# Optimization experiments

Measured on AMD Instinct MI355X. Metric: run time of the kernel, lower is better.

Reference implementation:

```python
import jax, jax.numpy as jnp
import numpy as np

HEADS = 12
DIM_HEAD = 64
PATCHES = 196  # tokens_to_attend (space attention)
DIM = 768
BATCH = 8
FRAMES = 16
TOKENS = FRAMES * PATCHES + 1  # + CLS


def setup_inputs() -> dict:
    key = jax.random.key(0)
    k1, k2, k3 = jax.random.split(key, 3)
    x = jax.random.normal(k1, (BATCH, TOKENS, DIM), dtype=jnp.float32)
    # small init scale keeps softmax logits in a sane range
    W_qkv = jax.random.normal(k2, (DIM, 3 * HEADS * DIM_HEAD), dtype=jnp.float32) * 0.02
    W_0 = jax.random.normal(k3, (HEADS * DIM_HEAD, DIM), dtype=jnp.float32) * 0.02
    return {"x": x, "W_qkv": W_qkv, "W_0": W_0}


def _mhsa(q, k, v, scale):
    # q: [g,h,i,d], k/v: [g,h,j,d]
    s = jnp.einsum('ghid,ghjd->ghij', q, k) * scale
    a = jax.nn.softmax(s, axis=-1)
    return jnp.einsum('ghij,ghjd->ghid', a, v)


def reference(x, W_qkv, W_0):
    b, t, _ = x.shape
    h, dh, p = HEADS, DIM_HEAD, PATCHES
    scale = dh ** -0.5

    qkv = x @ W_qkv  # [b,t,dh*3*h], flattened in (d, k, h) order per einops pattern
    qkv = qkv.reshape(b, t, dh, 3, h)
    q = jnp.transpose(qkv[:, :, :, 0, :], (0, 3, 1, 2))  # [b,h,t,d]
    k = jnp.transpose(qkv[:, :, :, 1, :], (0, 3, 1, 2))
    v = jnp.transpose(qkv[:, :, :, 2, :], (0, 3, 1, 2))

    # CLS query attends over ALL space-time tokens
    cls_q, q3 = q[:, :, :1], q[:, :, 1:]
    out_cls = _mhsa(cls_q, k, v, scale)  # [b,h,1,d]

    cls_k, k3 = k[:, :, :1], k[:, :, 1:]
    cls_v, v3 = v[:, :, :1], v[:, :, 1:]

    f = (t - 1) // p  # frames

    def space_rearrange(z):  # 'b h (f p) d -> (b f) h p d'
        z = z.reshape(b, h, f, p, dh)
        return jnp.transpose(z, (0, 2, 1, 3, 4)).reshape(b * f, h, p, dh)

    q_sep = space_rearrange(q3)
    k_sep = space_rearrange(k3)
    v_sep = space_rearrange(v3)

    # broadcast CLS key/value to every frame group: 'b ... -> (b tile) ...'
    cls_k = jnp.repeat(cls_k, f, axis=0)  # [b*f,h,1,d]
    cls_v = jnp.repeat(cls_v, f, axis=0)

    kk = jnp.concatenate((cls_k, k_sep), axis=2)  # [b*f,h,p+1,d]
    vv = jnp.concatenate((cls_v, v_sep), axis=2)

    out_sp = _mhsa(q_sep, kk, vv, scale)  # [b*f,h,p,d]

    # merge: '(b f) h p d -> b h (f p) d' (space=True path)
    out_sp = out_sp.reshape(b, f, h, p, dh)
    out_sp = jnp.transpose(out_sp, (0, 2, 1, 3, 4)).reshape(b, h, f * p, dh)

    out = jnp.concatenate((out_cls, out_sp), axis=2)  # [b,h,t,d]
    out = jnp.transpose(out, (0, 2, 1, 3)).reshape(b, t, h * dh)
    return out @ W_0
```

## Files before the change

### kernel.cpp

```cpp
#include <hip/hip_runtime.h>
#include <hip/hip_bf16.h>
#include <cstdint>

typedef unsigned short u16;
typedef uint32_t u32;
typedef __attribute__((ext_vector_type(8))) u16 u16x8;
typedef __attribute__((ext_vector_type(4))) u16 u16x4;
typedef __attribute__((ext_vector_type(8))) __bf16 bf16x8;
typedef __attribute__((ext_vector_type(4))) float f32x4;

#define B_    8
#define T_    3137
#define H_    12
#define F_    16
#define D_    768
#define M1    25096
#define VSTR  3200
#define NSPL  16
#define SPK   208

__device__ __forceinline__ u16 f2bf(float f) {
  unsigned u = __float_as_uint(f);
  return (u16)((u + 0x7FFFu + ((u >> 16) & 1u)) >> 16);
}
__device__ __forceinline__ float b2f(u16 v) {
  return __uint_as_float(((unsigned)v) << 16);
}

#define GLL(g, l) __builtin_amdgcn_global_load_lds( \
    (const __attribute__((address_space(1))) void*)(g), \
    (__attribute__((address_space(3))) void*)(l), 16, 0, 0)

__device__ __forceinline__ void dsr(bf16x8& d, u32 abyte) {
  asm volatile("ds_read_b128 %0, %1" : "=v"(d) : "v"(abyte));
}

#define BARR  __builtin_amdgcn_s_barrier()
#define LGKM0 asm volatile("s_waitcnt lgkmcnt(0)")
#define SCB   __builtin_amdgcn_sched_barrier(0)
#define PRI1  __builtin_amdgcn_s_setprio(1)
#define PRI0  __builtin_amdgcn_s_setprio(0)

__global__ __launch_bounds__(256) void k_cvt_x(const float* __restrict__ x,
                                               u16* __restrict__ xb, int n4) {
  int i = blockIdx.x * 256 + threadIdx.x;
  if (i >= n4) return;
  float4 v = ((const float4*)x)[i];
  u16x4 o = { f2bf(v.x), f2bf(v.y), f2bf(v.z), f2bf(v.w) };
  *(u16x4*)(xb + (size_t)i * 4) = o;
}

__global__ __launch_bounds__(256) void k_transpose(const float* __restrict__ in,
                                                   u16* __restrict__ out,
                                                   int R, int C, int qkvperm) {
  __shared__ float tile[32][33];
  int c0 = blockIdx.x * 32, r0 = blockIdx.y * 32;
  int tx = threadIdx.x, ty = threadIdx.y;
  #pragma unroll
  for (int i = ty; i < 32; i += 8)
    tile[i][tx] = in[(size_t)(r0 + i) * C + c0 + tx];
  __syncthreads();
  #pragma unroll
  for (int i = ty; i < 32; i += 8) {
    int c = c0 + i;
    int orow;
    if (qkvperm) {
      int d = c / 36, rem = c - d * 36;
      int comp = rem / 12, hh = rem - comp * 12;
      orow = comp * 768 + hh * 64 + d;
    } else {
      orow = c;
    }
    out[(size_t)orow * R + r0 + tx] = f2bf(tile[tx][i]);
  }
}

template<int EPI, int NX>
__global__ __launch_bounds__(256, 2) void k_gemm(const u16* __restrict__ A,
                                                 const u16* __restrict__ Bm,
                                                 float* __restrict__ outF,
                                                 u16* __restrict__ Qb,
                                                 u16* __restrict__ Kb,
                                                 u16* __restrict__ Vt) {
  __shared__ u16 lds[32768];
  const int tid = threadIdx.x;
  const int lane = tid & 63;
  const int wid = tid >> 6;
  const int wr = wid >> 1, wc = wid & 1;
  const int li = lane & 15, lg = lane >> 4;

  const int nwg = NX * 197;
  const int q = nwg >> 3, r = nwg & 7;
  const int g = blockIdx.x;
  const int xcd = g & 7, pos = g >> 3;
  const int s = ((xcd < r) ? xcd * (q + 1) : r * (q + 1) + (xcd - r) * q) + pos;
  const int arow0 = (s / NX) * 128;
  const int brow0 = (s % NX) * 128;

  const int srow = wid * 32 + (lane >> 3);
  const int scol = ((lane & 7) ^ (lane >> 3)) * 8;
  const u16* gA = A  + (size_t)(arow0 + srow) * 768 + scol;
  const u16* gB = Bm + (size_t)(brow0 + srow) * 768 + scol;

  const u32 ldsb = (u32)(uintptr_t)(__attribute__((address_space(3))) u16*)(&lds[0]);
  const u32 e0 = (u32)((lg ^ (li & 7)) * 16);
  const u32 e1 = (u32)(((lg + 4) ^ (li & 7)) * 16);
  const u32 aA = ldsb + (u32)(wr * 64 + li) * 128;
  const u32 aB = ldsb + 16384 + (u32)(wc * 64 + li) * 128;

  f32x4 acc[4][4] = {};

#define STAGE(TB, KS) do { const int kb_ = (KS) * 64; \
    _Pragma("unroll") for (int c_ = 0; c_ < 4; ++c_) { \
      GLL(gA + kb_ + c_ * 8 * 768, lds + (TB) * 16384 + wid * 2048 + c_ * 512); \
      GLL(gB + kb_ + c_ * 8 * 768, lds + (TB) * 16384 + 8192 + wid * 2048 + c_ * 512); \
    } \
  } while (0)

#define STEP(CUR, KV) do { \
    { const int ks_ = ((KV) + 1 < 12) ? (KV) + 1 : 11; STAGE((CUR) ^ 1, ks_); } \
    asm volatile("s_waitcnt vmcnt(8)"); \
    BARR; \
    bf16x8 af[4][2], bfr[4][2]; \
    _Pragma("unroll") for (int m = 0; m < 4; ++m) { \
      dsr(af[m][0], aA + (CUR) * 32768 + m * 2048 + e0); \
      dsr(af[m][1], aA + (CUR) * 32768 + m * 2048 + e1); } \
    _Pragma("unroll") for (int n = 0; n < 4; ++n) { \
      dsr(bfr[n][0], aB + (CUR) * 32768 + n * 2048 + e0); \
      dsr(bfr[n][1], aB + (CUR) * 32768 + n * 2048 + e1); } \
    LGKM0; SCB; PRI1; \
    _Pragma("unroll") for (int m = 0; m < 4; ++m) \
    _Pragma("unroll") for (int n = 0; n < 4; ++n) { \
      acc[m][n] = __builtin_amdgcn_mfma_f32_16x16x32_bf16(af[m][0], bfr[n][0], acc[m][n], 0, 0, 0); \
      acc[m][n] = __builtin_amdgcn_mfma_f32_16x16x32_bf16(af[m][1], bfr[n][1], acc[m][n], 0, 0, 0); } \
    PRI0; BARR; \
  } while (0)

  STAGE(0, 0);

  #pragma unroll 1
  for (int kk = 0; kk < 12; kk += 2) {
    STEP(0, kk);
    STEP(1, kk + 1);
  }
#undef STAGE
#undef STEP

  if (EPI == 0) {
    #pragma unroll
    for (int m = 0; m < 4; ++m)
      #pragma unroll
      for (int n = 0; n < 4; ++n) {
        const int colp = brow0 + wc * 64 + n * 16 + li;
        #pragma unroll
        for (int rr = 0; rr < 4; ++rr) {
          const int row = arow0 + wr * 64 + m * 16 + lg * 4 + rr;
          if (row < M1)
            __builtin_nontemporal_store(acc[m][n][rr], outF + (size_t)row * 768 + colp);
        }
      }
  } else {
    const int comp = brow0 / 768;
    const float qsc = (comp == 0) ? 0.125f : 1.0f;
    const int b0r = arow0 / T_;
    const int RB = (b0r + 1) * T_;
    __syncthreads();
    if (comp < 2) {
      u16* tl = &lds[0];
      #pragma unroll
      for (int m = 0; m < 4; ++m)
        #pragma unroll
        for (int n = 0; n < 4; ++n)
          #pragma unroll
          for (int rr = 0; rr < 4; ++rr)
            tl[(wr * 64 + m * 16 + lg * 4 + rr) * 136 + wc * 64 + n * 16 + li] =
                f2bf(acc[m][n][rr] * qsc);
      __syncthreads();
      u16* dst = (comp == 0) ? Qb : Kb;
      const int hh0 = (brow0 - comp * 768) >> 6;
      const int grp = tid >> 4, li2 = tid & 15;
      #pragma unroll
      for (int pass = 0; pass < 16; ++pass) {
        const int idx = pass * 16 + grp;
        const int row = idx >> 1, hl = idx & 1;
        const int rg = arow0 + row;
        if (rg >= M1) continue;
        const int bb = (rg >= RB) ? b0r + 1 : b0r;
        const int tt = rg - bb * T_;
        const size_t bh = (size_t)bb * H_ + hh0 + hl;
        *(u16x4*)(dst + ((bh * T_ + tt) << 6) + li2 * 4) =
            *(const u16x4*)(tl + row * 136 + hl * 64 + li2 * 4);
      }
    } else {
      u16* tl = &lds[0];
      #pragma unroll
      for (int m = 0; m < 4; ++m)
        #pragma unroll
        for (int n = 0; n < 4; ++n)
          #pragma unroll
          for (int rr = 0; rr < 4; ++rr)
            tl[(wr * 64 + m * 16 + lg * 4 + rr) * 130 + wc * 64 + n * 16 + li] =
                f2bf(acc[m][n][rr]);
      __syncthreads();
      const int vcol0 = brow0 - 1536;
      #pragma unroll 1
      for (int cc = 0; cc < 32; ++cc) {
        const int c = wid * 32 + cc;
        const int vcol = vcol0 + c;
        const int hh = vcol >> 6, dd = vcol & 63;
        #pragma unroll
        for (int half = 0; half < 2; ++half) {
          const int tloc = half * 64 + lane;
          const int rg = arow0 + tloc;
          if (rg >= M1) continue;
          const int bb = (rg >= RB) ? b0r + 1 : b0r;
          const int tt = rg - bb * T_;
          Vt[(((size_t)bb * H_ + hh) * 64 + dd) * VSTR + tt] = tl[tloc * 130 + c];
        }
      }
    }
  }
}

__global__ __launch_bounds__(512, 4) void k_attn_sp(const u16* __restrict__ Qb,
                                                    const u16* __restrict__ Kb,
                                                    const u16* __restrict__ Vt,
                                                    u16* __restrict__ AO) {
  __shared__ u16 Ks[224 * 64];
  __shared__ u16 Vs[4 * 64 * 64];
  __shared__ u16 P[8][16 * 72];
  const int bid = blockIdx.x;
  const int h = bid % H_;
  const int f = (bid / H_) % F_;
  const int b = bid / (H_ * F_);
  const int tid = threadIdx.x;
  const int lane = tid & 63, w = tid >> 6;
  const int li = lane & 15, lg = lane >> 4;
  const size_t bh = (size_t)b * H_ + h;
  const u16* Qp = Qb + bh * T_ * 64;
  const u16* Kp = Kb + bh * T_ * 64;
  const u16* Vp = Vt + bh * 64 * VSTR;
  u16* ps = &P[w][0];

  if (w < 7) {
    #pragma unroll
    for (int p = 0; p < 4; ++p) {
      const int c = (w * 4 + p) * 64 + lane;
      const int key = c >> 3, sp = lane & 7;
      const int tok = (key == 0) ? 0 : f * 196 + key;
      GLL(Kp + (size_t)tok * 64 + ((sp ^ (key & 7)) * 8), Ks + c * 8);
    }
  }
  {
    const int d = tid & 63, kg = (tid >> 6) & 3, sh = tid >> 8;
    #pragma unroll
    for (int st = 0; st < 2; ++st) {
      const int stt = sh + st * 2;
      const u16* src = Vp + (size_t)d * VSTR + f * 196 + stt * 64 + kg * 16;
      u16x4 a0 = *(const u16x4*)(src);
      u16x4 a1 = *(const u16x4*)(src + 4);
      u16x4 a2 = *(const u16x4*)(src + 8);
      u16x4 a3 = *(const u16x4*)(src + 12);
      if (stt == 0 && kg == 0) a0[0] = Vp[(size_t)d * VSTR];
      u16* row = Vs + stt * 4096 + d * 64;
      const int s0 = (kg * 2) ^ (d & 7), s1 = (kg * 2 + 1) ^ (d & 7);
      u16x8 w0 = { a0[0], a0[1], a0[2], a0[3], a1[0], a1[1], a1[2], a1[3] };
      u16x8 w1 = { a2[0], a2[1], a2[2], a2[3], a3[0], a3[1], a3[2], a3[3] };
      *(u16x8*)(row + s0 * 8) = w0;
      *(u16x8*)(row + s1 * 8) = w1;
    }
  }
  __syncthreads();

  for (int mt = w; mt < 13; mt += 8) {
    const int pp = mt * 16 + li;
    const int ppc = pp < 196 ? pp : 195;
    const size_t tq = 1 + f * 196 + ppc;
    const bf16x8 qf0 = *(const bf16x8*)(Qp + tq * 64 + lg * 8);
    const bf16x8 qf1 = *(const bf16x8*)(Qp + tq * 64 + 32 + lg * 8);

    f32x4 s[14] = {};
    #pragma unroll
    for (int n = 0; n < 14; ++n) {
      const int key = n * 16 + li;
      const u16* kp = Ks + key * 64;
      const bf16x8 kf0 = *(const bf16x8*)(kp + ((lg ^ (li & 7)) * 8));
      const bf16x8 kf1 = *(const bf16x8*)(kp + (((lg + 4) ^ (li & 7)) * 8));
      s[n] = __builtin_amdgcn_mfma_f32_16x16x32_bf16(qf0, kf0, s[n], 0, 0, 0);
      s[n] = __builtin_amdgcn_mfma_f32_16x16x32_bf16(qf1, kf1, s[n], 0, 0, 0);
    }

    float mx[4];
    #pragma unroll
    for (int r = 0; r < 4; ++r) {
      float m0 = -1e30f;
      #pragma unroll
      for (int n = 0; n < 14; ++n) {
        const int key = n * 16 + li;
        m0 = fmaxf(m0, (key < 197) ? s[n][r] : -1e30f);
      }
      #pragma unroll
      for (int msk = 1; msk < 16; msk <<= 1) m0 = fmaxf(m0, __shfl_xor(m0, msk));
      mx[r] = m0;
    }

    float rsum[4] = {0.f, 0.f, 0.f, 0.f};
    f32x4 o[4] = {};
    #pragma unroll
    for (int ks = 0; ks < 7; ++ks) {
      const int cofs = (ks & 1) * 32;
      #pragma unroll
      for (int half = 0; half < 2; ++half) {
        const int n = ks * 2 + half;
        const int key = n * 16 + li;
        #pragma unroll
        for (int r = 0; r < 4; ++r) {
          float p = (key < 197) ? __expf(s[n][r] - mx[r]) : 0.f;
          rsum[r] += p;
          ps[(lg * 4 + r) * 72 + cofs + half * 16 + li] = f2bf(p);
        }
      }
      asm volatile("s_waitcnt lgkmcnt(0)" ::: "memory");
      const bf16x8 pf = *(const bf16x8*)(ps + li * 72 + cofs + lg * 8);
      const int slot = ((ks & 1) * 4 + lg);
      #pragma unroll
      for (int n = 0; n < 4; ++n) {
        const int d = n * 16 + li;
        const bf16x8 vf = *(const bf16x8*)(Vs + (ks >> 1) * 4096 + d * 64 +
                                           ((slot ^ (li & 7)) * 8));
        o[n] = __builtin_amdgcn_mfma_f32_16x16x32_bf16(pf, vf, o[n], 0, 0, 0);
      }
    }

    #pragma unroll
    for (int r = 0; r < 4; ++r) {
      float su = rsum[r];
      #pragma unroll
      for (int msk = 1; msk < 16; msk <<= 1) su += __shfl_xor(su, msk);
      rsum[r] = su;
    }

    asm volatile("s_waitcnt lgkmcnt(0)" ::: "memory");
    #pragma unroll
    for (int n = 0; n < 4; ++n)
      #pragma unroll
      for (int r = 0; r < 4; ++r)
        ps[(lg * 4 + r) * 64 + n * 16 + li] = f2bf(o[n][r] / rsum[r]);
    asm volatile("s_waitcnt lgkmcnt(0)" ::: "memory");
    #pragma unroll
    for (int p2 = 0; p2 < 2; ++p2) {
      const int row = p2 * 8 + (lane >> 3);
      const int ch = lane & 7;
      const int ppo = mt * 16 + row;
      if (ppo < 196) {
        const size_t t = 1 + (size_t)f * 196 + ppo;
        *(u16x8*)(AO + ((size_t)b * T_ + t) * 768 + h * 64 + ch * 8) =
            *(const u16x8*)(ps + row * 64 + ch * 8);
      }
    }
  }
}

__global__ __launch_bounds__(256) void k_attn_cls1(const u16* __restrict__ Qb,
                                                   const u16* __restrict__ Kb,
                                                   const u16* __restrict__ Vt,
                                                   float* __restrict__ Pc) {
  __shared__ float qs[64];
  __shared__ float sv[SPK];
  __shared__ float red[8];
  const int bid = blockIdx.x;
  const int s = bid & (NSPL - 1);
  const int bh = bid >> 4;
  const u16* Qp = Qb + (size_t)bh * T_ * 64;
  const u16* Kp = Kb + (size_t)bh * T_ * 64;
  const u16* Vp = Vt + (size_t)bh * 64 * VSTR;
  const int base = s * SPK;
  const int nk0 = T_ - base;
  const int nk = (nk0 < SPK) ? nk0 : SPK;
  const int tid = threadIdx.x;
  const int lane = tid & 63, w = tid >> 6;

  if (tid < 64) qs[tid] = b2f(Qp[tid]);
  for (int jj = nk + tid; jj < SPK; jj += 256) sv[jj] = 0.f;
  __syncthreads();

  float lmax = -1e30f;
  for (int jj = tid; jj < nk; jj += 256) {
    const u16* kp = Kp + (size_t)(base + jj) * 64;
    float acc = 0.f;
    #pragma unroll
    for (int d0 = 0; d0 < 64; d0 += 8) {
      u16x8 kv = *(const u16x8*)(kp + d0);
      #pragma unroll
      for (int e = 0; e < 8; ++e) acc += qs[d0 + e] * b2f(kv[e]);
    }
    sv[jj] = acc;
    lmax = fmaxf(lmax, acc);
  }
  #pragma unroll
  for (int msk = 32; msk; msk >>= 1) lmax = fmaxf(lmax, __shfl_xor(lmax, msk));
  if (lane == 0) red[w] = lmax;
  __syncthreads();
  const float bmax = fmaxf(fmaxf(red[0], red[1]), fmaxf(red[2], red[3]));

  float lsum = 0.f;
  for (int jj = tid; jj < nk; jj += 256) {
    float p = __expf(sv[jj] - bmax);
    sv[jj] = p;
    lsum += p;
  }
  #pragma unroll
  for (int msk = 32; msk; msk >>= 1) lsum += __shfl_xor(lsum, msk);
  if (lane == 0) red[4 + w] = lsum;
  __syncthreads();
  const float bsum = red[4] + red[5] + red[6] + red[7];

  const int d = tid >> 2, q4 = tid & 3;
  const u16* vp = Vp + (size_t)d * VSTR + base + q4 * (SPK / 4);
  const float* sp = &sv[q4 * (SPK / 4)];
  float o = 0.f;
  #pragma unroll
  for (int k4 = 0; k4 < SPK / 4; k4 += 4) {
    u16x4 vv = *(const u16x4*)(vp + k4);
    o += sp[k4]     * b2f(vv[0]) + sp[k4 + 1] * b2f(vv[1])
       + sp[k4 + 2] * b2f(vv[2]) + sp[k4 + 3] * b2f(vv[3]);
  }
  o += __shfl_xor(o, 1);
  o += __shfl_xor(o, 2);

  float* P = Pc + ((size_t)bh * NSPL + s) * 66;
  if (tid == 0) { P[0] = bmax; P[1] = bsum; }
  if (q4 == 0) P[2 + d] = o;
}

__global__ __launch_bounds__(64) void k_attn_cls2(const float* __restrict__ Pc,
                                                  u16* __restrict__ AO) {
  const int bh = blockIdx.x;
  const int d = threadIdx.x;
  const float* P = Pc + (size_t)bh * NSPL * 66;
  float m = -1e30f;
  #pragma unroll
  for (int s = 0; s < NSPL; ++s) m = fmaxf(m, P[s * 66]);
  float l = 0.f, o = 0.f;
  #pragma unroll
  for (int s = 0; s < NSPL; ++s) {
    const float wgt = __expf(P[s * 66] - m);
    l += wgt * P[s * 66 + 1];
    o += wgt * P[s * 66 + 2 + d];
  }
  const int b = bh / H_, h = bh - b * H_;
  AO[(size_t)b * T_ * 768 + h * 64 + d] = f2bf(o / l);
}

extern "C" void kernel_launch(void* const* d_in, const int* in_sizes, int n_in,
                              void* d_out, int out_size, void* d_ws, size_t ws_size,
                              hipStream_t stream) {
  const float* x    = (const float*)d_in[0];
  const float* Wqkv = (const float*)d_in[1];
  const float* W0   = (const float*)d_in[2];
  float* out = (float*)d_out;
  char* ws = (char*)d_ws;

  u16* xb    = (u16*)(ws);
  u16* wqkvT = (u16*)(ws + 38731776);
  u16* w0T   = (u16*)(ws + 42270720);
  u16* Qb    = (u16*)(ws + 43450368);
  u16* Kb    = (u16*)(ws + 81997824);
  u16* Vt    = (u16*)(ws + 120545280);
  u16* AO = xb;
  float* Pc = (float*)wqkvT;

  k_cvt_x<<<dim3(18822), dim3(256), 0, stream>>>(x, xb, (M1 * D_) / 4);
  k_transpose<<<dim3(72, 24), dim3(32, 8), 0, stream>>>(Wqkv, wqkvT, 768, 2304, 1);
  k_transpose<<<dim3(24, 24), dim3(32, 8), 0, stream>>>(W0, w0T, 768, 768, 0);
  k_gemm<1, 18><<<dim3(18 * 197), dim3(256), 0, stream>>>(xb, wqkvT, nullptr, Qb, Kb, Vt);
  k_attn_sp<<<dim3(1536), dim3(512), 0, stream>>>(Qb, Kb, Vt, AO);
  k_attn_cls1<<<dim3(96 * NSPL), dim3(256), 0, stream>>>(Qb, Kb, Vt, Pc);
  k_attn_cls2<<<dim3(96), dim3(64), 0, stream>>>(Pc, AO);
  k_gemm<0, 6><<<dim3(6 * 197), dim3(256), 0, stream>>>(AO, w0T, out, nullptr, nullptr, nullptr);
}
```

Baseline: 252.9 us.

## Fuse fp32-to-bf16 conversion of x into the QKV GEMM A-tile load

Measured after the change: 386.8 us. +52.9%, slower.

```diff
diff --git a/kernel.cpp b/kernel.cpp
--- a/kernel.cpp
+++ b/kernel.cpp
@@ -41,15 +41,6 @@
 #define PRI1  __builtin_amdgcn_s_setprio(1)
 #define PRI0  __builtin_amdgcn_s_setprio(0)
 
-__global__ __launch_bounds__(256) void k_cvt_x(const float* __restrict__ x,
-                                               u16* __restrict__ xb, int n4) {
-  int i = blockIdx.x * 256 + threadIdx.x;
-  if (i >= n4) return;
-  float4 v = ((const float4*)x)[i];
-  u16x4 o = { f2bf(v.x), f2bf(v.y), f2bf(v.z), f2bf(v.w) };
-  *(u16x4*)(xb + (size_t)i * 4) = o;
-}
-
 __global__ __launch_bounds__(256) void k_transpose(const float* __restrict__ in,
                                                    u16* __restrict__ out,
                                                    int R, int C, int qkvperm) {
@@ -75,13 +66,11 @@
   }
 }
 
-template<int EPI, int NX>
-__global__ __launch_bounds__(256, 2) void k_gemm(const u16* __restrict__ A,
-                                                 const u16* __restrict__ Bm,
-                                                 float* __restrict__ outF,
-                                                 u16* __restrict__ Qb,
-                                                 u16* __restrict__ Kb,
-                                                 u16* __restrict__ Vt) {
+__global__ __launch_bounds__(256, 2) void k_gemm1(const float* __restrict__ X,
+                                                  const u16* __restrict__ Bm,
+                                                  u16* __restrict__ Qb,
+                                                  u16* __restrict__ Kb,
+                                                  u16* __restrict__ Vt) {
   __shared__ u16 lds[32768];
   const int tid = threadIdx.x;
   const int lane = tid & 63;
@@ -89,13 +78,174 @@
   const int wr = wid >> 1, wc = wid & 1;
   const int li = lane & 15, lg = lane >> 4;
 
-  const int nwg = NX * 197;
+  const int nwg = 18 * 197;
   const int q = nwg >> 3, r = nwg & 7;
   const int g = blockIdx.x;
   const int xcd = g & 7, pos = g >> 3;
   const int s = ((xcd < r) ? xcd * (q + 1) : r * (q + 1) + (xcd - r) * q) + pos;
-  const int arow0 = (s / NX) * 128;
-  const int brow0 = (s % NX) * 128;
+  const int arow0 = (s / 18) * 128;
+  const int brow0 = (s % 18) * 128;
+
+  const int arow = tid >> 1;
+  const int hh32 = (tid & 1) * 32;
+  int raG = arow0 + arow; if (raG >= M1) raG = M1 - 1;
+  const float* xA = X + (size_t)raG * 768 + hh32;
+  const u32 wrbase = (u32)arow * 64;
+
+  const int srow = wid * 32 + (lane >> 3);
+  const int scol = ((lane & 7) ^ (lane >> 3)) * 8;
+  const u16* gB = Bm + (size_t)(brow0 + srow) * 768 + scol;
+
+  const u32 ldsb = (u32)(uintptr_t)(__attribute__((address_space(3))) u16*)(&lds[0]);
+  const u32 e0 = (u32)((lg ^ (li & 7)) * 16);
+  const u32 e1 = (u32)(((lg + 4) ^ (li & 7)) * 16);
+  const u32 aA = ldsb + (u32)(wr * 64 + li) * 128;
+  const u32 aB = ldsb + 16384 + (u32)(wc * 64 + li) * 128;
+
+  f32x4 acc[4][4] = {};
+  float4 avA[8], avB[8];
+
+#define LOADA(AV, KS) do { const int kb_ = (KS) * 64; \
+    _Pragma("unroll") for (int j_ = 0; j_ < 8; ++j_) \
+      AV[j_] = *(const float4*)(xA + kb_ + j_ * 4); \
+  } while (0)
+
+#define WRA(AV, TB) do { \
+    _Pragma("unroll") for (int c_ = 0; c_ < 4; ++c_) { \
+      const float4 u0_ = AV[c_ * 2], u1_ = AV[c_ * 2 + 1]; \
+      u16x8 w_ = { f2bf(u0_.x), f2bf(u0_.y), f2bf(u0_.z), f2bf(u0_.w), \
+                   f2bf(u1_.x), f2bf(u1_.y), f2bf(u1_.z), f2bf(u1_.w) }; \
+      const int ch_ = hh32 / 8 + c_; \
+      *(u16x8*)(lds + (TB) * 16384 + wrbase + (u32)((ch_ ^ (arow & 7)) * 8)) = w_; \
+    } \
+  } while (0)
+
+#define STAGE_B(TB, KS) do { const int kb_ = (KS) * 64; \
+    _Pragma("unroll") for (int c_ = 0; c_ < 4; ++c_) \
+      GLL(gB + kb_ + c_ * 8 * 768, lds + (TB) * 16384 + 8192 + wid * 2048 + c_ * 512); \
+  } while (0)
+
+#define STEP(CUR, KV, AVC, AVN) do { \
+    { const int k1_ = ((KV) + 1 < 12) ? (KV) + 1 : 11; STAGE_B((CUR) ^ 1, k1_); } \
+    { const int k2_ = ((KV) + 2 < 12) ? (KV) + 2 : 11; LOADA(AVN, k2_); } \
+    bf16x8 af[4][2], bfr[4][2]; \
+    _Pragma("unroll") for (int m = 0; m < 4; ++m) { \
+      dsr(af[m][0], aA + (CUR) * 32768 + m * 2048 + e0); \
+      dsr(af[m][1], aA + (CUR) * 32768 + m * 2048 + e1); } \
+    _Pragma("unroll") for (int n = 0; n < 4; ++n) { \
+      dsr(bfr[n][0], aB + (CUR) * 32768 + n * 2048 + e0); \
+      dsr(bfr[n][1], aB + (CUR) * 32768 + n * 2048 + e1); } \
+    LGKM0; SCB; PRI1; \
+    _Pragma("unroll") for (int m = 0; m < 4; ++m) \
+    _Pragma("unroll") for (int n = 0; n < 4; ++n) { \
+      acc[m][n] = __builtin_amdgcn_mfma_f32_16x16x32_bf16(af[m][0], bfr[n][0], acc[m][n], 0, 0, 0); \
+      acc[m][n] = __builtin_amdgcn_mfma_f32_16x16x32_bf16(af[m][1], bfr[n][1], acc[m][n], 0, 0, 0); } \
+    PRI0; SCB; \
+    asm volatile("s_waitcnt vmcnt(12)"); \
+    WRA(AVC, (CUR) ^ 1); \
+    asm volatile("s_waitcnt vmcnt(8)"); \
+    LGKM0; \
+    BARR; \
+  } while (0)
+
+  LOADA(avA, 0);
+  asm volatile("s_waitcnt vmcnt(0)");
+  WRA(avA, 0);
+  STAGE_B(0, 0);
+  LOADA(avA, 1);
+  asm volatile("s_waitcnt vmcnt(8)");
+  LGKM0;
+  BARR;
+
+  #pragma unroll 1
+  for (int kk = 0; kk < 12; kk += 2) {
+    STEP(0, kk,     avA, avB);
+    STEP(1, kk + 1, avB, avA);
+  }
+#undef LOADA
+#undef WRA
+#undef STAGE_B
+#undef STEP
+
+  asm volatile("s_waitcnt vmcnt(0)");
+  const int comp = brow0 / 768;
+  const float qsc = (comp == 0) ? 0.125f : 1.0f;
+  const int b0r = arow0 / T_;
+  const int RB = (b0r + 1) * T_;
+  __syncthreads();
+  if (comp < 2) {
+    u16* tl = &lds[0];
+    #pragma unroll
+    for (int m = 0; m < 4; ++m)
+      #pragma unroll
+      for (int n = 0; n < 4; ++n)
+        #pragma unroll
+        for (int rr = 0; rr < 4; ++rr)
+          tl[(wr * 64 + m * 16 + lg * 4 + rr) * 136 + wc * 64 + n * 16 + li] =
+              f2bf(acc[m][n][rr] * qsc);
+    __syncthreads();
+    u16* dst = (comp == 0) ? Qb : Kb;
+    const int hh0 = (brow0 - comp * 768) >> 6;
+    const int grp = tid >> 4, li2 = tid & 15;
+    #pragma unroll
+    for (int pass = 0; pass < 16; ++pass) {
+      const int idx = pass * 16 + grp;
+      const int row = idx >> 1, hl = idx & 1;
+      const int rg = arow0 + row;
+      if (rg >= M1) continue;
+      const int bb = (rg >= RB) ? b0r + 1 : b0r;
+      const int tt = rg - bb * T_;
+      const size_t bh = (size_t)bb * H_ + hh0 + hl;
+      *(u16x4*)(dst + ((bh * T_ + tt) << 6) + li2 * 4) =
+          *(const u16x4*)(tl + row * 136 + hl * 64 + li2 * 4);
+    }
+  } else {
+    u16* tl = &lds[0];
+    #pragma unroll
+    for (int m = 0; m < 4; ++m)
+      #pragma unroll
+      for (int n = 0; n < 4; ++n)
+        #pragma unroll
+        for (int rr = 0; rr < 4; ++rr)
+          tl[(wr * 64 + m * 16 + lg * 4 + rr) * 130 + wc * 64 + n * 16 + li] =
+              f2bf(acc[m][n][rr]);
+    __syncthreads();
+    const int vcol0 = brow0 - 1536;
+    #pragma unroll 1
+    for (int cc = 0; cc < 32; ++cc) {
+      const int c = wid * 32 + cc;
+      const int vcol = vcol0 + c;
+      const int hh = vcol >> 6, dd = vcol & 63;
+      #pragma unroll
+      for (int half = 0; half < 2; ++half) {
+        const int tloc = half * 64 + lane;
+        const int rg = arow0 + tloc;
+        if (rg >= M1) continue;
+        const int bb = (rg >= RB) ? b0r + 1 : b0r;
+        const int tt = rg - bb * T_;
+        Vt[(((size_t)bb * H_ + hh) * 64 + dd) * VSTR + tt] = tl[tloc * 130 + c];
+      }
+    }
+  }
+}
+
+__global__ __launch_bounds__(256, 2) void k_gemmB(const u16* __restrict__ A,
+                                                  const u16* __restrict__ Bm,
+                                                  float* __restrict__ outF) {
+  __shared__ u16 lds[32768];
+  const int tid = threadIdx.x;
+  const int lane = tid & 63;
+  const int wid = tid >> 6;
+  const int wr = wid >> 1, wc = wid & 1;
+  const int li = lane & 15, lg = lane >> 4;
+
+  const int nwg = 6 * 197;
+  const int q = nwg >> 3, r = nwg & 7;
+  const int g = blockIdx.x;
+  const int xcd = g & 7, pos = g >> 3;
+  const int s = ((xcd < r) ? xcd * (q + 1) : r * (q + 1) + (xcd - r) * q) + pos;
+  const int arow0 = (s / 6) * 128;
+  const int brow0 = (s % 6) * 128;
 
   const int srow = wid * 32 + (lane >> 3);
   const int scol = ((lane & 7) ^ (lane >> 3)) * 8;
@@ -146,80 +296,18 @@
 #undef STAGE
 #undef STEP
 
-  if (EPI == 0) {
-    #pragma unroll
-    for (int m = 0; m < 4; ++m)
-      #pragma unroll
-      for (int n = 0; n < 4; ++n) {
-        const int colp = brow0 + wc * 64 + n * 16 + li;
-        #pragma unroll
-        for (int rr = 0; rr < 4; ++rr) {
-          const int row = arow0 + wr * 64 + m * 16 + lg * 4 + rr;
-          if (row < M1)
-            __builtin_nontemporal_store(acc[m][n][rr], outF + (size_t)row * 768 + colp);
-        }
+  #pragma unroll
+  for (int m = 0; m < 4; ++m)
+    #pragma unroll
+    for (int n = 0; n < 4; ++n) {
+      const int colp = brow0 + wc * 64 + n * 16 + li;
+      #pragma unroll
+      for (int rr = 0; rr < 4; ++rr) {
+        const int row = arow0 + wr * 64 + m * 16 + lg * 4 + rr;
+        if (row < M1)
+          __builtin_nontemporal_store(acc[m][n][rr], outF + (size_t)row * 768 + colp);
       }
-  } else {
-    const int comp = brow0 / 768;
-    const float qsc = (comp == 0) ? 0.125f : 1.0f;
-    const int b0r = arow0 / T_;
-    const int RB = (b0r + 1) * T_;
-    __syncthreads();
-    if (comp < 2) {
-      u16* tl = &lds[0];
-      #pragma unroll
-      for (int m = 0; m < 4; ++m)
-        #pragma unroll
-        for (int n = 0; n < 4; ++n)
-          #pragma unroll
-          for (int rr = 0; rr < 4; ++rr)
-            tl[(wr * 64 + m * 16 + lg * 4 + rr) * 136 + wc * 64 + n * 16 + li] =
-                f2bf(acc[m][n][rr] * qsc);
-      __syncthreads();
-      u16* dst = (comp == 0) ? Qb : Kb;
-      const int hh0 = (brow0 - comp * 768) >> 6;
-      const int grp = tid >> 4, li2 = tid & 15;
-      #pragma unroll
-      for (int pass = 0; pass < 16; ++pass) {
-        const int idx = pass * 16 + grp;
-        const int row = idx >> 1, hl = idx & 1;
-        const int rg = arow0 + row;
-        if (rg >= M1) continue;
-        const int bb = (rg >= RB) ? b0r + 1 : b0r;
-        const int tt = rg - bb * T_;
-        const size_t bh = (size_t)bb * H_ + hh0 + hl;
-        *(u16x4*)(dst + ((bh * T_ + tt) << 6) + li2 * 4) =
-            *(const u16x4*)(tl + row * 136 + hl * 64 + li2 * 4);
-      }
-    } else {
-      u16* tl = &lds[0];
-      #pragma unroll
-      for (int m = 0; m < 4; ++m)
-        #pragma unroll
-        for (int n = 0; n < 4; ++n)
-          #pragma unroll
-          for (int rr = 0; rr < 4; ++rr)
-            tl[(wr * 64 + m * 16 + lg * 4 + rr) * 130 + wc * 64 + n * 16 + li] =
-                f2bf(acc[m][n][rr]);
-      __syncthreads();
-      const int vcol0 = brow0 - 1536;
-      #pragma unroll 1
-      for (int cc = 0; cc < 32; ++cc) {
-        const int c = wid * 32 + cc;
-        const int vcol = vcol0 + c;
-        const int hh = vcol >> 6, dd = vcol & 63;
-        #pragma unroll
-        for (int half = 0; half < 2; ++half) {
-          const int tloc = half * 64 + lane;
-          const int rg = arow0 + tloc;
-          if (rg >= M1) continue;
-          const int bb = (rg >= RB) ? b0r + 1 : b0r;
-          const int tt = rg - bb * T_;
-          Vt[(((size_t)bb * H_ + hh) * 64 + dd) * VSTR + tt] = tl[tloc * 130 + c];
-        }
-      }
-    }
-  }
+    }
 }
 
 __global__ __launch_bounds__(512, 4) void k_attn_sp(const u16* __restrict__ Qb,
@@ -461,21 +549,19 @@
   float* out = (float*)d_out;
   char* ws = (char*)d_ws;
 
-  u16* xb    = (u16*)(ws);
+  u16* AO    = (u16*)(ws);
   u16* wqkvT = (u16*)(ws + 38731776);
   u16* w0T   = (u16*)(ws + 42270720);
   u16* Qb    = (u16*)(ws + 43450368);
   u16* Kb    = (u16*)(ws + 81997824);
   u16* Vt    = (u16*)(ws + 120545280);
-  u16* AO = xb;
   float* Pc = (float*)wqkvT;
 
-  k_cvt_x<<<dim3(18822), dim3(256), 0, stream>>>(x, xb, (M1 * D_) / 4);
   k_transpose<<<dim3(72, 24), dim3(32, 8), 0, stream>>>(Wqkv, wqkvT, 768, 2304, 1);
   k_transpose<<<dim3(24, 24), dim3(32, 8), 0, stream>>>(W0, w0T, 768, 768, 0);
-  k_gemm<1, 18><<<dim3(18 * 197), dim3(256), 0, stream>>>(xb, wqkvT, nullptr, Qb, Kb, Vt);
+  k_gemm1<<<dim3(18 * 197), dim3(256), 0, stream>>>(x, wqkvT, Qb, Kb, Vt);
   k_attn_sp<<<dim3(1536), dim3(512), 0, stream>>>(Qb, Kb, Vt, AO);
   k_attn_cls1<<<dim3(96 * NSPL), dim3(256), 0, stream>>>(Qb, Kb, Vt, Pc);
   k_attn_cls2<<<dim3(96), dim3(64), 0, stream>>>(Pc, AO);
-  k_gemm<0, 6><<<dim3(6 * 197), dim3(256), 0, stream>>>(AO, w0T, out, nullptr, nullptr, nullptr);
-}
+  k_gemmB<<<dim3(6 * 197), dim3(256), 0, stream>>>(AO, w0T, out);
+}
```
